# Performance work log

Hardware: AMD Instinct MI355X
Metric: run time of the kernel (lower is better)

Reference implementation:

```python
import jax, jax.numpy as jnp
import numpy as np

B, S, D_MODEL, NHEAD = 1, 512, 512, 8
D_K = D_MODEL // NHEAD
EPS = 1e-6


def _linear(x, w, b):
    # torch nn.Linear: x @ W^T + b
    return x @ w.T + b


def setup_inputs() -> dict:
    key = jax.random.key(0)
    ks = jax.random.split(key, 18)
    inp = {}
    for i, nm in enumerate(["query", "key", "value", "query_sigma", "key_sigma", "value_sigma"]):
        inp[nm] = jax.random.normal(ks[i], (B, S, D_MODEL), dtype=jnp.float32)
    bound = 1.0 / np.sqrt(D_MODEL)
    pnames = ["wq_mu", "bq_mu", "wk_mu", "bk_mu", "wv_mu", "bv_mu",
              "wq_s", "bq_s", "wk_s", "bk_s", "wv_s", "bv_s"]
    for i, nm in enumerate(pnames):
        shape = (D_MODEL, D_MODEL) if nm.startswith("w") else (D_MODEL,)
        inp[nm] = jax.random.uniform(ks[6 + i], shape, dtype=jnp.float32,
                                     minval=-bound, maxval=bound)
    return inp


def reference(query, key, value, query_sigma, key_sigma, value_sigma,
              wq_mu, bq_mu, wk_mu, bk_mu, wv_mu, bv_mu,
              wq_s, bq_s, wk_s, bk_s, wv_s, bv_s):
    b, s, _ = query.shape
    h, dk = NHEAD, D_K
    mu_q = _linear(query, wq_mu, bq_mu).reshape(b, s, h, dk)
    mu_k = _linear(key, wk_mu, bk_mu).reshape(b, s, h, dk)
    mu_v = _linear(value, wv_mu, bv_mu).reshape(b, s, h, dk)
    sg_q = _linear(query_sigma, wq_s, bq_s).reshape(b, s, h, dk)
    sg_k = _linear(key_sigma, wk_s, bk_s).reshape(b, s, h, dk)
    sg_v = _linear(value_sigma, wv_s, bv_s).reshape(b, s, h, dk)

    # Bhattacharyya distance: broadcast to [b, s_q, s_k, h, dk] then reduce dk
    a = sg_q[:, :, None] ** 2 + EPS   # [b, sq, 1, h, dk]
    c = sg_k[:, None, :] ** 2 + EPS   # [b, 1, sk, h, dk]
    term1 = 0.25 * jnp.log(0.25 * (a / c + c / a + 2.0))
    dmu = mu_q[:, :, None] - mu_k[:, None, :]
    term2 = 0.25 * dmu ** 2 / (sg_q[:, :, None] ** 2 + sg_k[:, None, :] ** 2 + EPS)
    dist = (term1 + term2).sum(-1) / np.sqrt(dk)  # [b, sq, sk, h]
    dist = dist.transpose(0, 3, 1, 2)             # [b, h, sq, sk]

    causal = jnp.triu(jnp.ones((s, s), dtype=bool), k=1)
    dist = jnp.where(causal[None, None], -jnp.inf, dist)
    attn = jax.nn.softmax(dist, axis=-1)

    out_mu = jnp.einsum('bhqk,bkhd->bhqd', attn, mu_v)
    out_var = jnp.maximum(jnp.einsum('bhqk,bkhd->bhqd', attn, sg_v ** 2), 0.0)
    out_sigma = jnp.sqrt(out_var + EPS)
    return out_mu, out_sigma
```

## Files before the change

### kernel.cpp

```cpp
#include <hip/hip_runtime.h>
#include <hip/hip_bf16.h>
#include <math.h>

#define SEQ 512
#define DM 512
#define NH 8
#define DKH 64
#define EPSV 1e-6f
#define LN2F 0.6931471805599453f

typedef __attribute__((ext_vector_type(8))) short short8v;
typedef __attribute__((ext_vector_type(8))) unsigned short ushort8v;
typedef __attribute__((ext_vector_type(16))) float f32x16;

__device__ inline unsigned short f2bf(float x) {
  union { float f; unsigned u; } v; v.f = x;
  unsigned r = v.u + 0x7FFFu + ((v.u >> 16) & 1u);
  return (unsigned short)(r >> 16);
}
__device__ inline float bf2f(unsigned short h) {
  union { float f; unsigned u; } v; v.u = ((unsigned)h) << 16;
  return v.f;
}

struct ConvArgs { const float* src[12]; };

__global__ __launch_bounds__(256) void convert_kernel(ConvArgs a,
                                                      unsigned short* __restrict__ pack) {
  const int m = blockIdx.x >> 7;
  const int g = ((blockIdx.x & 127) << 8) + threadIdx.x;
  const int r = g & 31, ko = (g >> 5) & 63, p = g >> 11;
  const float* src = a.src[m] + (p * 32 + r) * DM + ko * 8;
  float4 x0 = *(const float4*)src;
  float4 x1 = *(const float4*)(src + 4);
  float xs[8] = {x0.x, x0.y, x0.z, x0.w, x1.x, x1.y, x1.z, x1.w};
  ushort8v h1, h2, h3;
#pragma unroll
  for (int e = 0; e < 8; ++e) {
    unsigned short a1 = f2bf(xs[e]);
    float r1 = xs[e] - bf2f(a1);
    unsigned short a2 = f2bf(r1);
    float r2 = r1 - bf2f(a2);
    h1[e] = a1; h2[e] = a2; h3[e] = f2bf(r2);
  }
  unsigned short* dh = pack + (size_t)m * 786432 + p * 16384 + ko * 256 + r * 8;
  *(ushort8v*)dh = h1;
  *(ushort8v*)(dh + 262144) = h2;
  *(ushort8v*)(dh + 524288) = h3;
}

struct GemmArgs { const float* bias[6]; float* out[6]; };

__global__ __launch_bounds__(512) void mfma_proj_kernel(const unsigned short* __restrict__ pack,
                                                        GemmArgs ga) {
  const int p = blockIdx.z;
  const int by = blockIdx.y, bx = blockIdx.x;
  const int t = threadIdx.x, l = t & 63, w = t >> 6;
  const int qd = w & 3, kh = w >> 2;
  const int rowblk = qd >> 1, colblk = qd & 1;
  const int r = l & 31, koff = l >> 5;

  const unsigned short* A = pack + (size_t)p * 786432;
  const unsigned short* B = pack + (size_t)(6 + p) * 786432;
  const int pa = by * 2 + rowblk, pb = bx * 2 + colblk;
  const int ko0 = kh * 32 + koff;
  const size_t aoff = (size_t)pa * 16384 + (size_t)ko0 * 256 + r * 8;
  const size_t boff = (size_t)pb * 16384 + (size_t)ko0 * 256 + r * 8;
  const short8v* A1 = (const short8v*)(A + aoff);
  const short8v* A2 = (const short8v*)(A + 262144 + aoff);
  const short8v* A3 = (const short8v*)(A + 524288 + aoff);
  const short8v* B1 = (const short8v*)(B + boff);
  const short8v* B2 = (const short8v*)(B + 262144 + boff);
  const short8v* B3 = (const short8v*)(B + 524288 + boff);

  f32x16 acc = {};
#pragma unroll 2
  for (int s = 0; s < 16; ++s) {
    short8v a1 = A1[(size_t)s * 64];
    short8v a2 = A2[(size_t)s * 64];
    short8v a3 = A3[(size_t)s * 64];
    short8v b1 = B1[(size_t)s * 64];
    short8v b2 = B2[(size_t)s * 64];
    short8v b3 = B3[(size_t)s * 64];
    acc = __builtin_amdgcn_mfma_f32_32x32x16_bf16(a1, b1, acc, 0, 0, 0);
    acc = __builtin_amdgcn_mfma_f32_32x32x16_bf16(a2, b1, acc, 0, 0, 0);
    acc = __builtin_amdgcn_mfma_f32_32x32x16_bf16(a1, b2, acc, 0, 0, 0);
    acc = __builtin_amdgcn_mfma_f32_32x32x16_bf16(a3, b1, acc, 0, 0, 0);
    acc = __builtin_amdgcn_mfma_f32_32x32x16_bf16(a2, b2, acc, 0, 0, 0);
    acc = __builtin_amdgcn_mfma_f32_32x32x16_bf16(a1, b3, acc, 0, 0, 0);
  }

  __shared__ float red[4][32][33];
  if (kh == 1) {
#pragma unroll
    for (int i = 0; i < 16; ++i) {
      int row = (i & 3) + 8 * (i >> 2) + 4 * (l >> 5);
      red[qd][row][r] = acc[i];
    }
  }
  __syncthreads();
  if (kh == 0) {
    const int colg = bx * 64 + colblk * 32 + r;
    const float bias = ga.bias[p][colg];
    float* C = ga.out[p];
    const int rowbase = by * 64 + rowblk * 32;
#pragma unroll
    for (int i = 0; i < 16; ++i) {
      int row = (i & 3) + 8 * (i >> 2) + 4 * (l >> 5);
      float v = acc[i] + red[qd][row][r] + bias;
      if (p >= 3) v = fmaf(v, v, (p == 5) ? 0.f : EPSV);
      C[(size_t)(rowbase + row) * DM + colg] = v;
    }
  }
}

__global__ __launch_bounds__(256) void dist_kernel(const float* __restrict__ aq,
                                                   const float* __restrict__ ak,
                                                   const float* __restrict__ mq,
                                                   const float* __restrict__ mk,
                                                   float* __restrict__ dist) {
  const int blk = blockIdx.x;
  const int h = blk / 72;
  const int tt = blk % 72;
  int qt = (int)sqrtf((float)tt);
  while ((qt + 1) * (qt + 2) <= tt) ++qt;
  while (qt * (qt + 1) > tt) --qt;
  const int kt = tt - qt * (qt + 1);

  __shared__ float aqs[64][68], mqs[64][68], aks[32][68], mks[32][68];
  __shared__ float lsum[96][2];
  const int t = threadIdx.x;
#pragma unroll
  for (int i = 0; i < 4; ++i) {
    int idx = t + 256 * i;
    int r = idx >> 4, c4 = idx & 15;
    int gq = (qt * 64 + r) * DM + h * 64 + c4 * 4;
    *(float4*)&aqs[r][c4 * 4] = *(const float4*)&aq[gq];
    *(float4*)&mqs[r][c4 * 4] = *(const float4*)&mq[gq];
  }
#pragma unroll
  for (int i = 0; i < 2; ++i) {
    int idx = t + 256 * i;
    int r = idx >> 4, c4 = idx & 15;
    int gk = (kt * 32 + r) * DM + h * 64 + c4 * 4;
    *(float4*)&aks[r][c4 * 4] = *(const float4*)&ak[gk];
    *(float4*)&mks[r][c4 * 4] = *(const float4*)&mk[gk];
  }
  __syncthreads();

  if (t < 192) {
    int row = t >> 1, par = t & 1;
    const float* src = (row < 64) ? &aqs[row][0] : &aks[row - 64][0];
    float s = 0.f;
#pragma unroll
    for (int d = 0; d < 32; ++d) s += __log2f(src[par * 32 + d]);
    lsum[row][par] = s;
  }
  __syncthreads();

  const int tq = t >> 4, tk = t & 15;
  float accl[4][2], acct[4][2];
#pragma unroll
  for (int i = 0; i < 4; ++i)
#pragma unroll
    for (int j = 0; j < 2; ++j) { accl[i][j] = 0.f; acct[i][j] = 0.f; }

#pragma unroll 2
  for (int d4 = 0; d4 < 16; ++d4) {
    float4 qa[4], qm[4], ka[2], km[2];
#pragma unroll
    for (int i = 0; i < 4; ++i) {
      qa[i] = *(const float4*)&aqs[tq * 4 + i][d4 * 4];
      qm[i] = *(const float4*)&mqs[tq * 4 + i][d4 * 4];
    }
#pragma unroll
    for (int j = 0; j < 2; ++j) {
      ka[j] = *(const float4*)&aks[tk + 16 * j][d4 * 4];
      km[j] = *(const float4*)&mks[tk + 16 * j][d4 * 4];
    }
#pragma unroll
    for (int i = 0; i < 4; ++i) {
      float qav[4] = {qa[i].x, qa[i].y, qa[i].z, qa[i].w};
      float qmv[4] = {qm[i].x, qm[i].y, qm[i].z, qm[i].w};
#pragma unroll
      for (int j = 0; j < 2; ++j) {
        float kav[4] = {ka[j].x, ka[j].y, ka[j].z, ka[j].w};
        float kmv[4] = {km[j].x, km[j].y, km[j].z, km[j].w};
#pragma unroll
        for (int e = 0; e < 4; ++e) {
          float s = qav[e] + kav[e];
          accl[i][j] += __log2f(s);
          float dm = qmv[e] - kmv[e];
          float rcp = __builtin_amdgcn_rcpf(s - EPSV);
          acct[i][j] = fmaf(dm * dm, rcp, acct[i][j]);
        }
      }
    }
  }

  const int qg0 = qt * 64 + tq * 4;
#pragma unroll
  for (int i = 0; i < 4; ++i) {
    float la2 = lsum[tq * 4 + i][0] + lsum[tq * 4 + i][1];
#pragma unroll
    for (int j = 0; j < 2; ++j) {
      int kg = kt * 32 + tk + 16 * j;
      float lc2 = lsum[64 + tk + 16 * j][0] + lsum[64 + tk + 16 * j][1];
      float dv = (LN2F * (0.5f * accl[i][j] - 0.25f * (la2 + lc2) - 32.f)
                  + 0.25f * acct[i][j]) * 0.125f;
      dist[((size_t)(h * SEQ) + qg0 + i) * SEQ + kg] = dv;
    }
  }
}

__global__ __launch_bounds__(256) void softmax_pvpack_kernel(const float* __restrict__ dist,
                                                             const float* __restrict__ mv,
                                                             const float* __restrict__ sv2,
                                                             unsigned short* __restrict__ aPack,
                                                             unsigned short* __restrict__ vPack) {
  __shared__ float tile[64][65];
  const int t = threadIdx.x;

  if (blockIdx.x < 1024) {
    const int wid = blockIdx.x * 4 + (t >> 6);
    const int l = t & 63;
    const int h = wid >> 9;
    const int q = wid & 511;
    const float* row = dist + (size_t)wid * SEQ;

    float4 v0 = *(const float4*)&row[l * 8];
    float4 v1 = *(const float4*)&row[l * 8 + 4];
    float vals[8] = {v0.x, v0.y, v0.z, v0.w, v1.x, v1.y, v1.z, v1.w};
    float m = -1e30f;
#pragma unroll
    for (int e = 0; e < 8; ++e) {
      vals[e] = (l * 8 + e <= q) ? vals[e] : -1e30f;
      m = fmaxf(m, vals[e]);
    }
#pragma unroll
    for (int o = 32; o; o >>= 1) m = fmaxf(m, __shfl_xor(m, o, 64));
    float ssum = 0.f;
#pragma unroll
    for (int e = 0; e < 8; ++e) {
      float p = (l * 8 + e <= q) ? __expf(vals[e] - m) : 0.f;
      vals[e] = p;
      ssum += p;
    }
#pragma unroll
    for (int o = 32; o; o >>= 1) ssum += __shfl_xor(ssum, o, 64);
    float rs = 1.f / ssum;

    ushort8v hi, lo;
#pragma unroll
    for (int e = 0; e < 8; ++e) {
      float p = vals[e] * rs;
      unsigned short hh = f2bf(p);
      hi[e] = hh;
      lo[e] = f2bf(p - bf2f(hh));
    }
    unsigned short* dst = aPack + (size_t)h * 524288 + (q >> 5) * 16384 + l * 256 + (q & 31) * 8;
    *(ushort8v*)dst = hi;
    *(ushort8v*)(dst + 262144) = lo;
  } else {
    const int bb = blockIdx.x - 1024;
    const int h = bb >> 1;
    const int mm = bb & 1;
    const float* src = (mm == 0) ? mv : sv2;
    unsigned short* base = vPack + (size_t)(h * 2 + mm) * 65536;

    for (int k0 = 0; k0 < SEQ; k0 += 64) {
      __syncthreads();
#pragma unroll
      for (int i = 0; i < 4; ++i) {
        int idx = t + 256 * i;
        int r = idx >> 4, c4 = idx & 15;
        float4 v = *(const float4*)&src[(size_t)(k0 + r) * DM + h * 64 + c4 * 4];
        tile[r][c4 * 4 + 0] = v.x; tile[r][c4 * 4 + 1] = v.y;
        tile[r][c4 * 4 + 2] = v.z; tile[r][c4 * 4 + 3] = v.w;
      }
      __syncthreads();
#pragma unroll
      for (int i = 0; i < 2; ++i) {
        int idx = t + 256 * i;
        int d = idx & 63, ko = idx >> 6;
        ushort8v hi, lo;
#pragma unroll
        for (int e = 0; e < 8; ++e) {
          float x = tile[ko * 8 + e][d];
          unsigned short hh = f2bf(x);
          hi[e] = hh;
          lo[e] = f2bf(x - bf2f(hh));
        }
        int koG = (k0 >> 3) + ko;
        unsigned short* dst = base + (d >> 5) * 16384 + koG * 256 + (d & 31) * 8;
        *(ushort8v*)dst = hi;
        *(ushort8v*)(dst + 32768) = lo;
      }
    }
  }
}

__global__ __launch_bounds__(256) void pv_mfma_kernel(const unsigned short* __restrict__ aPack,
                                                      const unsigned short* __restrict__ vPack,
                                                      float* __restrict__ out) {
  const int h = blockIdx.x >> 4;
  const int qt = blockIdx.x & 15;
  const int t = threadIdx.x, l = t & 63, w = t >> 6;
  const int dt = w & 1, mm = w >> 1;

  const unsigned short* aBase = aPack + (size_t)h * 524288 + qt * 16384
                                + (l >> 5) * 256 + (l & 31) * 8;
  const unsigned short* vBase = vPack + (size_t)(h * 2 + mm) * 65536 + dt * 16384
                                + (l >> 5) * 256 + (l & 31) * 8;

  f32x16 acc = {};
  const int nks = 2 * qt + 2;
  for (int s = 0; s < nks; ++s) {
    short8v a1 = *(const short8v*)(aBase + (size_t)s * 512);
    short8v a2 = *(const short8v*)(aBase + 262144 + (size_t)s * 512);
    short8v b1 = *(const short8v*)(vBase + (size_t)s * 512);
    short8v b2 = *(const short8v*)(vBase + 32768 + (size_t)s * 512);
    acc = __builtin_amdgcn_mfma_f32_32x32x16_bf16(a1, b1, acc, 0, 0, 0);
    acc = __builtin_amdgcn_mfma_f32_32x32x16_bf16(a2, b1, acc, 0, 0, 0);
    acc = __builtin_amdgcn_mfma_f32_32x32x16_bf16(a1, b2, acc, 0, 0, 0);
  }

  float* dst = out + ((mm == 0) ? 0 : (size_t)NH * SEQ * DKH);
  const int col = dt * 32 + (l & 31);
#pragma unroll
  for (int i = 0; i < 16; ++i) {
    int qrow = (i & 3) + 8 * (i >> 2) + 4 * (l >> 5);
    int q = qt * 32 + qrow;
    float v = acc[i];
    if (mm) v = sqrtf(fmaxf(v, 0.f) + EPSV);
    dst[((size_t)h * SEQ + q) * DKH + col] = v;
  }
}

extern "C" void kernel_launch(void* const* d_in, const int* in_sizes, int n_in,
                              void* d_out, int out_size, void* d_ws, size_t ws_size,
                              hipStream_t stream) {
  (void)in_sizes; (void)n_in; (void)out_size; (void)ws_size;

  float* ws = (float*)d_ws;
  float* mq = ws;
  float* mk = mq + 262144;
  float* mv = mk + 262144;
  float* sq = mv + 262144;
  float* sk = sq + 262144;
  float* sv = sk + 262144;
  unsigned short* pack = (unsigned short*)(sv + 262144);
  float* dist = (float*)pack;
  unsigned short* aPack = pack + 4194304;
  unsigned short* vPack = pack + 8388608;

  ConvArgs ca;
  ca.src[0] = (const float*)d_in[0];
  ca.src[1] = (const float*)d_in[1];
  ca.src[2] = (const float*)d_in[2];
  ca.src[3] = (const float*)d_in[3];
  ca.src[4] = (const float*)d_in[4];
  ca.src[5] = (const float*)d_in[5];
  ca.src[6] = (const float*)d_in[6];
  ca.src[7] = (const float*)d_in[8];
  ca.src[8] = (const float*)d_in[10];
  ca.src[9] = (const float*)d_in[12];
  ca.src[10] = (const float*)d_in[14];
  ca.src[11] = (const float*)d_in[16];

  GemmArgs gaArgs;
  gaArgs.bias[0] = (const float*)d_in[7];  gaArgs.out[0] = mq;
  gaArgs.bias[1] = (const float*)d_in[9];  gaArgs.out[1] = mk;
  gaArgs.bias[2] = (const float*)d_in[11]; gaArgs.out[2] = mv;
  gaArgs.bias[3] = (const float*)d_in[13]; gaArgs.out[3] = sq;
  gaArgs.bias[4] = (const float*)d_in[15]; gaArgs.out[4] = sk;
  gaArgs.bias[5] = (const float*)d_in[17]; gaArgs.out[5] = sv;

  convert_kernel<<<12 * 128, 256, 0, stream>>>(ca, pack);

  dim3 ggrid(8, 8, 6);
  mfma_proj_kernel<<<ggrid, 512, 0, stream>>>(pack, gaArgs);

  dist_kernel<<<8 * 72, 256, 0, stream>>>(sq, sk, mq, mk, dist);

  softmax_pvpack_kernel<<<1040, 256, 0, stream>>>(dist, mv, sv, aPack, vPack);

  pv_mfma_kernel<<<128, 256, 0, stream>>>(aPack, vPack, (float*)d_out);
}
```

Before: 166.8 us.

## Drop low-half of attention weights and swizzle block orders across kernels

Attention probabilities are now stored as a single bf16 value instead of a hi/lo split. This halves the aPack buffer and removes one MFMA per k-step in the PV kernel, at the cost of reduced precision on the attention weights. The projection, dist, softmax and PV kernels also remap block indices so that heads and projections are interleaved across consecutive blocks, probably to spread triangular work and memory traffic more evenly across CUs/XCDs. The PV loop is unrolled by two.

```diff
diff --git a/kernel.cpp b/kernel.cpp
--- a/kernel.cpp
+++ b/kernel.cpp
@@ -53,8 +53,11 @@
 
 __global__ __launch_bounds__(512) void mfma_proj_kernel(const unsigned short* __restrict__ pack,
                                                         GemmArgs ga) {
-  const int p = blockIdx.z;
-  const int by = blockIdx.y, bx = blockIdx.x;
+  const int bid = blockIdx.x;
+  const int swz = (bid & 7) * 48 + (bid >> 3);
+  const int p = swz >> 6;
+  const int rem = swz & 63;
+  const int by = rem >> 3, bx = rem & 7;
   const int t = threadIdx.x, l = t & 63, w = t >> 6;
   const int qd = w & 3, kh = w >> 2;
   const int rowblk = qd >> 1, colblk = qd & 1;
@@ -120,8 +123,8 @@
                                                    const float* __restrict__ mk,
                                                    float* __restrict__ dist) {
   const int blk = blockIdx.x;
-  const int h = blk / 72;
-  const int tt = blk % 72;
+  const int h = blk & 7;
+  const int tt = blk >> 3;
   int qt = (int)sqrtf((float)tt);
   while ((qt + 1) * (qt + 2) <= tt) ++qt;
   while (qt * (qt + 1) > tt) --qt;
@@ -222,11 +225,11 @@
   const int t = threadIdx.x;
 
   if (blockIdx.x < 1024) {
-    const int wid = blockIdx.x * 4 + (t >> 6);
+    const int h = blockIdx.x & 7;
+    const int qq = blockIdx.x >> 3;
+    const int q = qq * 4 + (t >> 6);
     const int l = t & 63;
-    const int h = wid >> 9;
-    const int q = wid & 511;
-    const float* row = dist + (size_t)wid * SEQ;
+    const float* row = dist + ((size_t)h * SEQ + q) * SEQ;
 
     float4 v0 = *(const float4*)&row[l * 8];
     float4 v1 = *(const float4*)&row[l * 8 + 4];
@@ -250,17 +253,11 @@
     for (int o = 32; o; o >>= 1) ssum += __shfl_xor(ssum, o, 64);
     float rs = 1.f / ssum;
 
-    ushort8v hi, lo;
-#pragma unroll
-    for (int e = 0; e < 8; ++e) {
-      float p = vals[e] * rs;
-      unsigned short hh = f2bf(p);
-      hi[e] = hh;
-      lo[e] = f2bf(p - bf2f(hh));
-    }
-    unsigned short* dst = aPack + (size_t)h * 524288 + (q >> 5) * 16384 + l * 256 + (q & 31) * 8;
+    ushort8v hi;
+#pragma unroll
+    for (int e = 0; e < 8; ++e) hi[e] = f2bf(vals[e] * rs);
+    unsigned short* dst = aPack + (size_t)h * 262144 + (q >> 5) * 16384 + l * 256 + (q & 31) * 8;
     *(ushort8v*)dst = hi;
-    *(ushort8v*)(dst + 262144) = lo;
   } else {
     const int bb = blockIdx.x - 1024;
     const int h = bb >> 1;
@@ -303,25 +300,24 @@
 __global__ __launch_bounds__(256) void pv_mfma_kernel(const unsigned short* __restrict__ aPack,
                                                       const unsigned short* __restrict__ vPack,
                                                       float* __restrict__ out) {
-  const int h = blockIdx.x >> 4;
-  const int qt = blockIdx.x & 15;
+  const int h = blockIdx.x & 7;
+  const int qt = blockIdx.x >> 3;
   const int t = threadIdx.x, l = t & 63, w = t >> 6;
   const int dt = w & 1, mm = w >> 1;
 
-  const unsigned short* aBase = aPack + (size_t)h * 524288 + qt * 16384
+  const unsigned short* aBase = aPack + (size_t)h * 262144 + qt * 16384
                                 + (l >> 5) * 256 + (l & 31) * 8;
   const unsigned short* vBase = vPack + (size_t)(h * 2 + mm) * 65536 + dt * 16384
                                 + (l >> 5) * 256 + (l & 31) * 8;
 
   f32x16 acc = {};
   const int nks = 2 * qt + 2;
+#pragma unroll 2
   for (int s = 0; s < nks; ++s) {
     short8v a1 = *(const short8v*)(aBase + (size_t)s * 512);
-    short8v a2 = *(const short8v*)(aBase + 262144 + (size_t)s * 512);
     short8v b1 = *(const short8v*)(vBase + (size_t)s * 512);
     short8v b2 = *(const short8v*)(vBase + 32768 + (size_t)s * 512);
     acc = __builtin_amdgcn_mfma_f32_32x32x16_bf16(a1, b1, acc, 0, 0, 0);
-    acc = __builtin_amdgcn_mfma_f32_32x32x16_bf16(a2, b1, acc, 0, 0, 0);
     acc = __builtin_amdgcn_mfma_f32_32x32x16_bf16(a1, b2, acc, 0, 0, 0);
   }
 
@@ -352,7 +348,7 @@
   unsigned short* pack = (unsigned short*)(sv + 262144);
   float* dist = (float*)pack;
   unsigned short* aPack = pack + 4194304;
-  unsigned short* vPack = pack + 8388608;
+  unsigned short* vPack = pack + 6291456;
 
   ConvArgs ca;
   ca.src[0] = (const float*)d_in[0];
@@ -378,8 +374,7 @@
 
   convert_kernel<<<12 * 128, 256, 0, stream>>>(ca, pack);
 
-  dim3 ggrid(8, 8, 6);
-  mfma_proj_kernel<<<ggrid, 512, 0, stream>>>(pack, gaArgs);
+  mfma_proj_kernel<<<384, 512, 0, stream>>>(pack, gaArgs);
 
   dist_kernel<<<8 * 72, 256, 0, stream>>>(sq, sk, mq, mk, dist);
 
```

Measured after the change: 173.1 us. +3.7%, slower.

## Batch log2 via products, skip masked loads, drop attention lo-split in PV

Applied to the files above, without the earlier changes.

The distance kernel now multiplies four variance sums and takes one log2 of the product instead of four separate log2 calls, in both the inner loop and the per-row lsum. Softmax skips loading fully masked chunks of each causal row. The attention probabilities are stored only as a single bf16 instead of a hi/lo split, which halves the aPack buffer and removes one MFMA per step in the PV kernel, and that loop is unrolled by two. The product trick risks fp32 underflow or overflow for extreme variances, and dropping the lo term lowers the precision of the attention weights.

```diff
diff --git a/kernel.cpp b/kernel.cpp
--- a/kernel.cpp
+++ b/kernel.cpp
@@ -153,7 +153,11 @@
     const float* src = (row < 64) ? &aqs[row][0] : &aks[row - 64][0];
     float s = 0.f;
 #pragma unroll
-    for (int d = 0; d < 32; ++d) s += __log2f(src[par * 32 + d]);
+    for (int d = 0; d < 32; d += 4) {
+      float pr = src[par * 32 + d] * src[par * 32 + d + 1]
+               * src[par * 32 + d + 2] * src[par * 32 + d + 3];
+      s += __log2f(pr);
+    }
     lsum[row][par] = s;
   }
   __syncthreads();
@@ -186,14 +190,16 @@
       for (int j = 0; j < 2; ++j) {
         float kav[4] = {ka[j].x, ka[j].y, ka[j].z, ka[j].w};
         float kmv[4] = {km[j].x, km[j].y, km[j].z, km[j].w};
+        float pr = 1.f;
 #pragma unroll
         for (int e = 0; e < 4; ++e) {
           float s = qav[e] + kav[e];
-          accl[i][j] += __log2f(s);
+          pr = (e == 0) ? s : pr * s;
           float dm = qmv[e] - kmv[e];
           float rcp = __builtin_amdgcn_rcpf(s - EPSV);
           acct[i][j] = fmaf(dm * dm, rcp, acct[i][j]);
         }
+        accl[i][j] += __log2f(pr);
       }
     }
   }
@@ -228,14 +234,21 @@
     const int q = wid & 511;
     const float* row = dist + (size_t)wid * SEQ;
 
-    float4 v0 = *(const float4*)&row[l * 8];
-    float4 v1 = *(const float4*)&row[l * 8 + 4];
-    float vals[8] = {v0.x, v0.y, v0.z, v0.w, v1.x, v1.y, v1.z, v1.w};
+    float vals[8];
     float m = -1e30f;
-#pragma unroll
-    for (int e = 0; e < 8; ++e) {
-      vals[e] = (l * 8 + e <= q) ? vals[e] : -1e30f;
-      m = fmaxf(m, vals[e]);
+    if (l * 8 <= q) {
+      float4 v0 = *(const float4*)&row[l * 8];
+      float4 v1 = *(const float4*)&row[l * 8 + 4];
+      vals[0] = v0.x; vals[1] = v0.y; vals[2] = v0.z; vals[3] = v0.w;
+      vals[4] = v1.x; vals[5] = v1.y; vals[6] = v1.z; vals[7] = v1.w;
+#pragma unroll
+      for (int e = 0; e < 8; ++e) {
+        vals[e] = (l * 8 + e <= q) ? vals[e] : -1e30f;
+        m = fmaxf(m, vals[e]);
+      }
+    } else {
+#pragma unroll
+      for (int e = 0; e < 8; ++e) vals[e] = -1e30f;
     }
 #pragma unroll
     for (int o = 32; o; o >>= 1) m = fmaxf(m, __shfl_xor(m, o, 64));
@@ -250,17 +263,11 @@
     for (int o = 32; o; o >>= 1) ssum += __shfl_xor(ssum, o, 64);
     float rs = 1.f / ssum;
 
-    ushort8v hi, lo;
-#pragma unroll
-    for (int e = 0; e < 8; ++e) {
-      float p = vals[e] * rs;
-      unsigned short hh = f2bf(p);
-      hi[e] = hh;
-      lo[e] = f2bf(p - bf2f(hh));
-    }
-    unsigned short* dst = aPack + (size_t)h * 524288 + (q >> 5) * 16384 + l * 256 + (q & 31) * 8;
+    ushort8v hi;
+#pragma unroll
+    for (int e = 0; e < 8; ++e) hi[e] = f2bf(vals[e] * rs);
+    unsigned short* dst = aPack + (size_t)h * 262144 + (q >> 5) * 16384 + l * 256 + (q & 31) * 8;
     *(ushort8v*)dst = hi;
-    *(ushort8v*)(dst + 262144) = lo;
   } else {
     const int bb = blockIdx.x - 1024;
     const int h = bb >> 1;
@@ -308,20 +315,19 @@
   const int t = threadIdx.x, l = t & 63, w = t >> 6;
   const int dt = w & 1, mm = w >> 1;
 
-  const unsigned short* aBase = aPack + (size_t)h * 524288 + qt * 16384
+  const unsigned short* aBase = aPack + (size_t)h * 262144 + qt * 16384
                                 + (l >> 5) * 256 + (l & 31) * 8;
   const unsigned short* vBase = vPack + (size_t)(h * 2 + mm) * 65536 + dt * 16384
                                 + (l >> 5) * 256 + (l & 31) * 8;
 
   f32x16 acc = {};
   const int nks = 2 * qt + 2;
+#pragma unroll 2
   for (int s = 0; s < nks; ++s) {
     short8v a1 = *(const short8v*)(aBase + (size_t)s * 512);
-    short8v a2 = *(const short8v*)(aBase + 262144 + (size_t)s * 512);
     short8v b1 = *(const short8v*)(vBase + (size_t)s * 512);
     short8v b2 = *(const short8v*)(vBase + 32768 + (size_t)s * 512);
     acc = __builtin_amdgcn_mfma_f32_32x32x16_bf16(a1, b1, acc, 0, 0, 0);
-    acc = __builtin_amdgcn_mfma_f32_32x32x16_bf16(a2, b1, acc, 0, 0, 0);
     acc = __builtin_amdgcn_mfma_f32_32x32x16_bf16(a1, b2, acc, 0, 0, 0);
   }
 
@@ -352,7 +358,7 @@
   unsigned short* pack = (unsigned short*)(sv + 262144);
   float* dist = (float*)pack;
   unsigned short* aPack = pack + 4194304;
-  unsigned short* vPack = pack + 8388608;
+  unsigned short* vPack = pack + 6291456;
 
   ConvArgs ca;
   ca.src[0] = (const float*)d_in[0];
```

New measurement: 159.8 us. 1.04x faster.
